# Kernel optimization log

Measured on AMD Instinct MI355X. Metric: run time of the kernel, lower is better.

Reference implementation:

```python
import jax, jax.numpy as jnp
import numpy as np

N_NODES = 50000
N_EDGES = 800000
IN_FEATS = 256
OUT_FEATS = 128


def setup_inputs() -> dict:
    key = jax.random.key(0)
    k1, k2, k3, k4 = jax.random.split(key, 4)
    feat = jax.random.normal(k1, (N_NODES, IN_FEATS), dtype=jnp.float32)
    # xavier uniform init for weight [in, out]
    limit = float(np.sqrt(6.0 / (IN_FEATS + OUT_FEATS)))
    weight = jax.random.uniform(k2, (IN_FEATS, OUT_FEATS), minval=-limit, maxval=limit, dtype=jnp.float32)
    bias = jnp.zeros((OUT_FEATS,), dtype=jnp.float32)
    src = jax.random.randint(k3, (N_EDGES,), 0, N_NODES, dtype=jnp.int32)
    dst = jax.random.randint(k4, (N_EDGES,), 0, N_NODES, dtype=jnp.int32)
    return {"feat": feat, "weight": weight, "bias": bias, "src": src, "dst": dst}


def reference(feat, weight, bias, src, dst):
    N = feat.shape[0]
    in_f, out_f = weight.shape
    # right normalization: 1 / out_degree(src node), clamped to >= 1
    deg = jax.ops.segment_sum(jnp.ones(src.shape[0], dtype=feat.dtype), src, num_segments=N)
    norm = (1.0 / jnp.maximum(deg, 1.0))[:, None]  # [N,1]
    if in_f > out_f:
        # transform first (cheaper messages), then normalize + aggregate
        h = jnp.matmul(feat, weight) * norm          # [N, out]
        rst = jax.ops.segment_sum(h[src], dst, num_segments=N)  # scatter-sum over edges
    else:
        h = feat * norm                               # [N, in]
        rst = jax.ops.segment_sum(h[src], dst, num_segments=N)
        rst = jnp.matmul(rst, weight)
    return rst + bias
```

## Files before the change

kernel.cpp:

```cpp
#include <hip/hip_runtime.h>

#define N_NODES 50000
#define N_EDGES 800000
#define IN_F 256
#define OUT_F 128

#define CHUNKS 128
#define EPC (N_EDGES / CHUNKS)
#define BINW (N_NODES / 4)
#define NWORDS (N_NODES / 4)
#define RGB 196
#define HIST_BLOCKS (2 * CHUNKS)
#define CPW8 (CHUNKS / 8)

#define GEMMF_BLOCKS 196
#define HEPC (EPC / 2)

typedef __attribute__((ext_vector_type(8))) short short8;
typedef __attribute__((ext_vector_type(4))) float float4_t;

__device__ __forceinline__ short f2bf(float f) {
  unsigned u = __builtin_bit_cast(unsigned, f);
  u = u + 0x7FFFu + ((u >> 16) & 1u);
  return (short)(u >> 16);
}

__device__ __forceinline__ float bflo(unsigned u) {
  return __builtin_bit_cast(float, u << 16);
}
__device__ __forceinline__ float bfhi(unsigned u) {
  return __builtin_bit_cast(float, u & 0xFFFF0000u);
}


__global__ __launch_bounds__(512) void hist_kernel(const int* __restrict__ src,
                                                   const int* __restrict__ dst,
                                                   unsigned char* __restrict__ pdst8,
                                                   unsigned char* __restrict__ psrc8,
                                                   unsigned char* __restrict__ rank8,
                                                   int* __restrict__ cursor) {
  __shared__ unsigned bins[BINW];
  int b = blockIdx.x;
  int tid = threadIdx.x;
  if (b == 0 && tid == 0) *cursor = 0;
  int hs = b >> 7;
  int c = b & 127;
  uint4* b4 = (uint4*)bins;
  for (int j = tid; j < BINW / 4; j += 512) b4[j] = (uint4){0u, 0u, 0u, 0u};
  __syncthreads();
  const int* key = hs ? src : dst;
  int e0 = c * EPC;

  auto process = [&](int v, int eI) {
    unsigned sh = (v & 3) * 8;
    unsigned old = atomicAdd(&bins[v >> 2], 1u << sh);
    if (!hs) rank8[eI] = (unsigned char)((old >> sh) & 0xFFu);
  };

#pragma unroll 2
  for (int tile = 0; tile < 3; ++tile) {
    int i = tile * 2048 + tid;
    int k0 = key[e0 + i];
    int k1 = key[e0 + i + 512];
    int k2 = key[e0 + i + 1024];
    int k3 = key[e0 + i + 1536];
    process(k0, e0 + i);
    process(k1, e0 + i + 512);
    process(k2, e0 + i + 1024);
    process(k3, e0 + i + 1536);
  }
  {
    int i = 6144 + tid;
    if (i < EPC) process(key[e0 + i], e0 + i);
  }
  __syncthreads();
  uint4* p128 = (uint4*)((hs ? psrc8 : pdst8) + (size_t)c * N_NODES);
  const uint4* s128 = (const uint4*)bins;
  for (int j = tid; j < BINW / 4; j += 512) p128[j] = s128[j];
}

__global__ __launch_bounds__(512) void gemmred_kernel(const float* __restrict__ feat,
                                                      const float* __restrict__ W,
                                                      unsigned short* __restrict__ h,
                                                      const unsigned char* __restrict__ pdst8,
                                                      const unsigned char* __restrict__ psrc8,
                                                      unsigned char* __restrict__ delta8,
                                                      int* __restrict__ cnt,
                                                      int* __restrict__ row_start,
                                                      int* __restrict__ cursor,
                                                      float* __restrict__ norm) {
  __shared__ uint4 smem4[4096];
  int b = blockIdx.x;
  int tid = threadIdx.x;

  if (b < GEMMF_BLOCKS) {
    short* wl = (short*)smem4;
#pragma unroll
    for (int i = 0; i < 64; ++i) {
      int idx = i * 512 + tid;
      int k = idx >> 7, n = idx & 127;
      int s = k >> 5, q = (k >> 3) & 3, j = k & 7;
      int tt = n >> 4, m = n & 15;
      wl[((s * 8 + tt) * 64 + q * 16 + m) * 8 + j] = f2bf(W[idx]);
    }
    __syncthreads();

    int w = tid >> 6, l = tid & 63;
    int m = l & 15, q = l >> 4;
    long base = (long)b * 256 + w * 32;

    float4_t acc[2][8];
#pragma unroll
    for (int r = 0; r < 2; ++r)
#pragma unroll
      for (int to = 0; to < 8; ++to) acc[r][to] = (float4_t)(0.0f);

    long row0 = base + m;
    long row1 = base + 16 + m;
    long r0c = row0 < N_NODES - 1 ? row0 : N_NODES - 1;
    long r1c = row1 < N_NODES - 1 ? row1 : N_NODES - 1;
    const float* a0p = feat + (size_t)r0c * IN_F;
    const float* a1p = feat + (size_t)r1c * IN_F;
    const short8* wl8 = (const short8*)smem4;

#pragma unroll
    for (int s = 0; s < 8; ++s) {
      int k0 = s * 32 + q * 8;
      float4_t av0a = *(const float4_t*)(a0p + k0);
      float4_t av0b = *(const float4_t*)(a0p + k0 + 4);
      float4_t av1a = *(const float4_t*)(a1p + k0);
      float4_t av1b = *(const float4_t*)(a1p + k0 + 4);
      short8 fa0, fa1;
#pragma unroll
      for (int i = 0; i < 4; ++i) {
        fa0[i] = f2bf(av0a[i]);
        fa0[i + 4] = f2bf(av0b[i]);
        fa1[i] = f2bf(av1a[i]);
        fa1[i + 4] = f2bf(av1b[i]);
      }
#pragma unroll
      for (int to = 0; to < 8; ++to) {
        short8 fb = wl8[(s * 8 + to) * 64 + l];
        acc[0][to] = __builtin_amdgcn_mfma_f32_16x16x32_bf16(fa0, fb, acc[0][to], 0, 0, 0);
        acc[1][to] = __builtin_amdgcn_mfma_f32_16x16x32_bf16(fa1, fb, acc[1][to], 0, 0, 0);
      }
    }

#pragma unroll
    for (int r = 0; r < 2; ++r) {
#pragma unroll
      for (int i = 0; i < 4; ++i) {
        long row = base + r * 16 + q * 4 + i;
        if (row < N_NODES) {
          short8 hv;
#pragma unroll
          for (int to = 0; to < 8; ++to) hv[to] = f2bf(acc[r][to][i]);
          *(short8*)(h + (size_t)row * OUT_F + m * 8) = hv;
        }
      }
    }
    return;
  }

  int rb = b - GEMMF_BLOCKS;
  int side = rb >= RGB ? 1 : 0;
  int g = rb - side * RGB;
  int w = tid >> 6, l = tid & 63;
  int wd = g * 64 + l;
  bool ok = wd < NWORDS;
  int wdc = ok ? wd : NWORDS - 1;
  const unsigned* P = (const unsigned*)(side == 0 ? pdst8 : psrc8);
  unsigned(*tot)[64] = (unsigned(*)[64])smem4;

  unsigned vals[CPW8];
  unsigned s = 0;
#pragma unroll
  for (int i = 0; i < CPW8; ++i) {
    vals[i] = P[(size_t)(w * CPW8 + i) * NWORDS + wdc];
    s += vals[i];
  }
  tot[w][l] = s;
  __syncthreads();

  if (side == 0) {
    unsigned base = 0;
#pragma unroll
    for (int w2 = 0; w2 < 8; ++w2)
      if (w2 < w) base += tot[w2][l];
    unsigned run = base;
    unsigned* D = (unsigned*)delta8;
    if (ok) {
#pragma unroll
      for (int i = 0; i < CPW8; ++i) {
        D[(size_t)(w * CPW8 + i) * NWORDS + wd] = run;
        run += vals[i];
      }
    }
    if (w == 0) {
      unsigned ftot = 0;
#pragma unroll
      for (int w2 = 0; w2 < 8; ++w2) ftot += tot[w2][l];
      if (!ok) ftot = 0;
      int c0 = ftot & 255, c1 = (ftot >> 8) & 255, c2 = (ftot >> 16) & 255, c3 = ftot >> 24;
      int T = c0 + c1 + c2 + c3;
      int x = T;
#pragma unroll
      for (int off = 1; off < 64; off <<= 1) {
        int y = __shfl_up(x, off);
        if (l >= off) x += y;
      }
      int waveTotal = __shfl(x, 63);
      int sb = 0;
      if (l == 63) sb = atomicAdd(cursor, waveTotal);
      sb = __shfl(sb, 63);
      int E = sb + x - T;
      if (ok) {
        int4 cv = {c0, c1, c2, c3};
        int4 rv = {E, E + c0, E + c0 + c1, E + c0 + c1 + c2};
        ((int4*)cnt)[wd] = cv;
        ((int4*)row_start)[wd] = rv;
      }
    }
  } else {
    if (w == 0 && ok) {
      unsigned ftot = 0;
#pragma unroll
      for (int w2 = 0; w2 < 8; ++w2) ftot += tot[w2][l];
      float4 nv;
      int d0 = ftot & 255, d1 = (ftot >> 8) & 255, d2 = (ftot >> 16) & 255, d3 = (int)(ftot >> 24);
      nv.x = 1.0f / (float)(d0 > 1 ? d0 : 1);
      nv.y = 1.0f / (float)(d1 > 1 ? d1 : 1);
      nv.z = 1.0f / (float)(d2 > 1 ? d2 : 1);
      nv.w = 1.0f / (float)(d3 > 1 ? d3 : 1);
      ((float4*)norm)[wd] = nv;
    }
  }
}

__global__ __launch_bounds__(512) void scat_kernel(const int* __restrict__ src,
                                                   const int* __restrict__ dst,
                                                   const int* __restrict__ row_start,
                                                   const unsigned char* __restrict__ delta8,
                                                   const unsigned char* __restrict__ rank8,
                                                   int* __restrict__ eidx) {
  __shared__ uint4 dl4[N_NODES / 16];
  int b = blockIdx.x;
  int tid = threadIdx.x;
  int c = b >> 1, hb = b & 1;
  const uint4* rowp = (const uint4*)(delta8 + (size_t)c * N_NODES);
  for (int j = tid; j < N_NODES / 16; j += 512) dl4[j] = rowp[j];
  __syncthreads();
  const unsigned char* dl = (const unsigned char*)dl4;
  int e0 = c * EPC + hb * HEPC;

  int dsts[6], rks[6], srcs[6], rss[6];
#pragma unroll
  for (int k = 0; k < 6; ++k) {
    int e = e0 + k * 512 + tid;
    dsts[k] = dst[e];
    rks[k] = (int)rank8[e];
  }
#pragma unroll
  for (int k = 0; k < 6; ++k) rss[k] = row_start[dsts[k]];
#pragma unroll
  for (int k = 0; k < 6; ++k) srcs[k] = src[e0 + k * 512 + tid];
#pragma unroll
  for (int k = 0; k < 6; ++k) {
    int pos = rss[k] + (int)dl[dsts[k]] + rks[k];
    eidx[pos] = srcs[k];
  }
  if (tid < HEPC - 6 * 512) {
    int e = e0 + 3072 + tid;
    int d = dst[e];
    int pos = row_start[d] + (int)dl[d] + (int)rank8[e];
    eidx[pos] = src[e];
  }
}

__global__ __launch_bounds__(256) void agg_kernel(const unsigned short* __restrict__ h,
                                                  const int* __restrict__ row_start,
                                                  const int* __restrict__ cnt,
                                                  const int* __restrict__ eidx,
                                                  const float* __restrict__ norm,
                                                  const float* __restrict__ bias,
                                                  float* __restrict__ out) {
  int w = threadIdx.x >> 6, l = threadIdx.x & 63;
  int d = blockIdx.x * 4 + w;
  int rs = row_start[d], re = rs + cnt[d];
  const uint4* __restrict__ hu4 = (const uint4*)h;
  int rowsel = l >> 4;
  int cp = l & 15;
  float a0 = 0.f, a1 = 0.f, a2 = 0.f, a3 = 0.f, a4 = 0.f, a5 = 0.f, a6 = 0.f, a7 = 0.f;

  auto acc8 = [&](uint4 v, float nm) {
    a0 = fmaf(bflo(v.x), nm, a0); a1 = fmaf(bfhi(v.x), nm, a1);
    a2 = fmaf(bflo(v.y), nm, a2); a3 = fmaf(bfhi(v.y), nm, a3);
    a4 = fmaf(bflo(v.z), nm, a4); a5 = fmaf(bfhi(v.z), nm, a5);
    a6 = fmaf(bflo(v.w), nm, a6); a7 = fmaf(bfhi(v.w), nm, a7);
  };

  for (int bse = rs; bse < re; bse += 64) {
    int n = re - bse; if (n > 64) n = 64;
    int e = (l < n) ? eidx[bse + l] : 0;
    int quarter = (n + 3) >> 2;
    int j = 0;
    for (; j + 4 <= quarter; j += 4) {
      int i0 = 4 * j + rowsel;
      int s0 = __shfl(e, i0);
      int s1 = __shfl(e, i0 + 4);
      int s2 = __shfl(e, i0 + 8);
      int s3 = __shfl(e, i0 + 12);
      uint4 v0 = hu4[(size_t)s0 * 16 + cp];
      uint4 v1 = hu4[(size_t)s1 * 16 + cp];
      uint4 v2 = hu4[(size_t)s2 * 16 + cp];
      uint4 v3 = hu4[(size_t)s3 * 16 + cp];
      float nm0 = norm[s0], nm1 = norm[s1], nm2 = norm[s2], nm3 = norm[s3];
      if (i0 >= n) v0 = (uint4){0u, 0u, 0u, 0u};
      if (i0 + 4 >= n) v1 = (uint4){0u, 0u, 0u, 0u};
      if (i0 + 8 >= n) v2 = (uint4){0u, 0u, 0u, 0u};
      if (i0 + 12 >= n) v3 = (uint4){0u, 0u, 0u, 0u};
      acc8(v0, nm0);
      acc8(v1, nm1);
      acc8(v2, nm2);
      acc8(v3, nm3);
    }
    for (; j < quarter; ++j) {
      int i0 = 4 * j + rowsel;
      int s0 = __shfl(e, i0);
      uint4 v0 = hu4[(size_t)s0 * 16 + cp];
      float nm0 = norm[s0];
      if (i0 >= n) v0 = (uint4){0u, 0u, 0u, 0u};
      acc8(v0, nm0);
    }
  }
  a0 += __shfl_xor(a0, 16); a1 += __shfl_xor(a1, 16);
  a2 += __shfl_xor(a2, 16); a3 += __shfl_xor(a3, 16);
  a4 += __shfl_xor(a4, 16); a5 += __shfl_xor(a5, 16);
  a6 += __shfl_xor(a6, 16); a7 += __shfl_xor(a7, 16);
  a0 += __shfl_xor(a0, 32); a1 += __shfl_xor(a1, 32);
  a2 += __shfl_xor(a2, 32); a3 += __shfl_xor(a3, 32);
  a4 += __shfl_xor(a4, 32); a5 += __shfl_xor(a5, 32);
  a6 += __shfl_xor(a6, 32); a7 += __shfl_xor(a7, 32);
  if (rowsel == 0) {
    float av[8] = {a0, a1, a2, a3, a4, a5, a6, a7};
    float* op = out + (size_t)d * OUT_F;
#pragma unroll
    for (int j = 0; j < 8; ++j) {
      int col = j * 16 + cp;
      op[col] = av[j] + bias[col];
    }
  }
}

extern "C" void kernel_launch(void* const* d_in, const int* in_sizes, int n_in,
                              void* d_out, int out_size, void* d_ws, size_t ws_size,
                              hipStream_t stream) {
  const float* feat = (const float*)d_in[0];
  const float* weight = (const float*)d_in[1];
  const float* bias = (const float*)d_in[2];
  const int* src = (const int*)d_in[3];
  const int* dst = (const int*)d_in[4];
  float* out = (float*)d_out;

  char* ws = (char*)d_ws;
  size_t off = 0;
  auto alloc = [&](size_t bytes) -> void* {
    void* p = ws + off;
    off += (bytes + 511) & ~(size_t)511;
    return p;
  };
  int* cursor = (int*)alloc(4);
  int* cnt = (int*)alloc(N_NODES * 4);
  int* row_start = (int*)alloc(N_NODES * 4);
  float* norm = (float*)alloc(N_NODES * 4);
  int* eidx = (int*)alloc(N_EDGES * 4);
  unsigned short* h = (unsigned short*)alloc((size_t)N_NODES * OUT_F * 2);
  unsigned char* pdst8 = (unsigned char*)alloc((size_t)CHUNKS * N_NODES);
  unsigned char* psrc8 = (unsigned char*)alloc((size_t)CHUNKS * N_NODES);
  unsigned char* delta8 = (unsigned char*)alloc((size_t)CHUNKS * N_NODES);
  unsigned char* rank8 = (unsigned char*)alloc((size_t)N_EDGES);
  (void)off; (void)ws_size; (void)in_sizes; (void)n_in; (void)out_size;

  hipLaunchKernelGGL(hist_kernel, dim3(HIST_BLOCKS), dim3(512), 0, stream,
                     src, dst, pdst8, psrc8, rank8, cursor);
  hipLaunchKernelGGL(gemmred_kernel, dim3(GEMMF_BLOCKS + 2 * RGB), dim3(512), 0, stream,
                     feat, weight, h, pdst8, psrc8, delta8, cnt, row_start, cursor, norm);
  hipLaunchKernelGGL(scat_kernel, dim3(2 * CHUNKS), dim3(512), 0, stream,
                     src, dst, row_start, delta8, rank8, eidx);
  hipLaunchKernelGGL(agg_kernel, dim3(N_NODES / 4), dim3(256), 0, stream,
                     h, row_start, cnt, eidx, norm, bias, out);
}
```

Before: 161.9 us.

## Split GEMM blocks across histogram and reduction kernels to overlap work

The dense feature GEMM blocks are moved into a shared device function. Half of them now run alongside the histogram blocks in the first kernel and the other half alongside the prefix-reduction blocks in the second kernel, instead of all running in the second kernel. This spreads compute-bound GEMM work over both launches so it can fill CUs left idle by the memory/atomic-bound histogram phase. The cost is that the histogram kernel now uses the larger 64KB shared-memory footprint, which may reduce its occupancy.

```diff
diff --git a/kernel.cpp b/kernel.cpp
--- a/kernel.cpp
+++ b/kernel.cpp
@@ -14,6 +14,8 @@
 #define CPW8 (CHUNKS / 8)
 
 #define GEMMF_BLOCKS 196
+#define GEMM_K1 98
+#define GEMM_K2 98
 #define HEPC (EPC / 2)
 
 typedef __attribute__((ext_vector_type(8))) short short8;
@@ -33,15 +35,97 @@
 }
 
 
-__global__ __launch_bounds__(512) void hist_kernel(const int* __restrict__ src,
-                                                   const int* __restrict__ dst,
-                                                   unsigned char* __restrict__ pdst8,
-                                                   unsigned char* __restrict__ psrc8,
-                                                   unsigned char* __restrict__ rank8,
-                                                   int* __restrict__ cursor) {
-  __shared__ unsigned bins[BINW];
+__device__ __forceinline__ void gemm_block(int gb, int tid,
+                                           const float* __restrict__ feat,
+                                           const float* __restrict__ W,
+                                           unsigned short* __restrict__ h,
+                                           uint4* smem4) {
+  short* wl = (short*)smem4;
+#pragma unroll
+  for (int i = 0; i < 64; ++i) {
+    int idx = i * 512 + tid;
+    int k = idx >> 7, n = idx & 127;
+    int s = k >> 5, q = (k >> 3) & 3, j = k & 7;
+    int tt = n >> 4, m = n & 15;
+    wl[((s * 8 + tt) * 64 + q * 16 + m) * 8 + j] = f2bf(W[idx]);
+  }
+  __syncthreads();
+
+  int w = tid >> 6, l = tid & 63;
+  int m = l & 15, q = l >> 4;
+  long base = (long)gb * 256 + w * 32;
+
+  float4_t acc[2][8];
+#pragma unroll
+  for (int r = 0; r < 2; ++r)
+#pragma unroll
+    for (int to = 0; to < 8; ++to) acc[r][to] = (float4_t)(0.0f);
+
+  long row0 = base + m;
+  long row1 = base + 16 + m;
+  long r0c = row0 < N_NODES - 1 ? row0 : N_NODES - 1;
+  long r1c = row1 < N_NODES - 1 ? row1 : N_NODES - 1;
+  const float* a0p = feat + (size_t)r0c * IN_F;
+  const float* a1p = feat + (size_t)r1c * IN_F;
+  const short8* wl8 = (const short8*)smem4;
+
+#pragma unroll
+  for (int s = 0; s < 8; ++s) {
+    int k0 = s * 32 + q * 8;
+    float4_t av0a = *(const float4_t*)(a0p + k0);
+    float4_t av0b = *(const float4_t*)(a0p + k0 + 4);
+    float4_t av1a = *(const float4_t*)(a1p + k0);
+    float4_t av1b = *(const float4_t*)(a1p + k0 + 4);
+    short8 fa0, fa1;
+#pragma unroll
+    for (int i = 0; i < 4; ++i) {
+      fa0[i] = f2bf(av0a[i]);
+      fa0[i + 4] = f2bf(av0b[i]);
+      fa1[i] = f2bf(av1a[i]);
+      fa1[i + 4] = f2bf(av1b[i]);
+    }
+#pragma unroll
+    for (int to = 0; to < 8; ++to) {
+      short8 fb = wl8[(s * 8 + to) * 64 + l];
+      acc[0][to] = __builtin_amdgcn_mfma_f32_16x16x32_bf16(fa0, fb, acc[0][to], 0, 0, 0);
+      acc[1][to] = __builtin_amdgcn_mfma_f32_16x16x32_bf16(fa1, fb, acc[1][to], 0, 0, 0);
+    }
+  }
+
+#pragma unroll
+  for (int r = 0; r < 2; ++r) {
+#pragma unroll
+    for (int i = 0; i < 4; ++i) {
+      long row = base + r * 16 + q * 4 + i;
+      if (row < N_NODES) {
+        short8 hv;
+#pragma unroll
+        for (int to = 0; to < 8; ++to) hv[to] = f2bf(acc[r][to][i]);
+        *(short8*)(h + (size_t)row * OUT_F + m * 8) = hv;
+      }
+    }
+  }
+}
+
+__global__ __launch_bounds__(512) void histgemm_kernel(const int* __restrict__ src,
+                                                       const int* __restrict__ dst,
+                                                       unsigned char* __restrict__ pdst8,
+                                                       unsigned char* __restrict__ psrc8,
+                                                       unsigned char* __restrict__ rank8,
+                                                       int* __restrict__ cursor,
+                                                       const float* __restrict__ feat,
+                                                       const float* __restrict__ W,
+                                                       unsigned short* __restrict__ h) {
+  __shared__ uint4 smem4[4096];
   int b = blockIdx.x;
   int tid = threadIdx.x;
+
+  if (b >= HIST_BLOCKS) {
+    gemm_block(b - HIST_BLOCKS, tid, feat, W, h, smem4);
+    return;
+  }
+
+  unsigned* bins = (unsigned*)smem4;
   if (b == 0 && tid == 0) *cursor = 0;
   int hs = b >> 7;
   int c = b & 127;
@@ -75,11 +159,11 @@
   }
   __syncthreads();
   uint4* p128 = (uint4*)((hs ? psrc8 : pdst8) + (size_t)c * N_NODES);
-  const uint4* s128 = (const uint4*)bins;
+  const uint4* s128 = (const uint4*)smem4;
   for (int j = tid; j < BINW / 4; j += 512) p128[j] = s128[j];
 }
 
-__global__ __launch_bounds__(512) void gemmred_kernel(const float* __restrict__ feat,
+__global__ __launch_bounds__(512) void redgemm_kernel(const float* __restrict__ feat,
                                                       const float* __restrict__ W,
                                                       unsigned short* __restrict__ h,
                                                       const unsigned char* __restrict__ pdst8,
@@ -93,78 +177,13 @@
   int b = blockIdx.x;
   int tid = threadIdx.x;
 
-  if (b < GEMMF_BLOCKS) {
-    short* wl = (short*)smem4;
-#pragma unroll
-    for (int i = 0; i < 64; ++i) {
-      int idx = i * 512 + tid;
-      int k = idx >> 7, n = idx & 127;
-      int s = k >> 5, q = (k >> 3) & 3, j = k & 7;
-      int tt = n >> 4, m = n & 15;
-      wl[((s * 8 + tt) * 64 + q * 16 + m) * 8 + j] = f2bf(W[idx]);
-    }
-    __syncthreads();
-
-    int w = tid >> 6, l = tid & 63;
-    int m = l & 15, q = l >> 4;
-    long base = (long)b * 256 + w * 32;
-
-    float4_t acc[2][8];
-#pragma unroll
-    for (int r = 0; r < 2; ++r)
-#pragma unroll
-      for (int to = 0; to < 8; ++to) acc[r][to] = (float4_t)(0.0f);
-
-    long row0 = base + m;
-    long row1 = base + 16 + m;
-    long r0c = row0 < N_NODES - 1 ? row0 : N_NODES - 1;
-    long r1c = row1 < N_NODES - 1 ? row1 : N_NODES - 1;
-    const float* a0p = feat + (size_t)r0c * IN_F;
-    const float* a1p = feat + (size_t)r1c * IN_F;
-    const short8* wl8 = (const short8*)smem4;
-
-#pragma unroll
-    for (int s = 0; s < 8; ++s) {
-      int k0 = s * 32 + q * 8;
-      float4_t av0a = *(const float4_t*)(a0p + k0);
-      float4_t av0b = *(const float4_t*)(a0p + k0 + 4);
-      float4_t av1a = *(const float4_t*)(a1p + k0);
-      float4_t av1b = *(const float4_t*)(a1p + k0 + 4);
-      short8 fa0, fa1;
-#pragma unroll
-      for (int i = 0; i < 4; ++i) {
-        fa0[i] = f2bf(av0a[i]);
-        fa0[i + 4] = f2bf(av0b[i]);
-        fa1[i] = f2bf(av1a[i]);
-        fa1[i + 4] = f2bf(av1b[i]);
-      }
-#pragma unroll
-      for (int to = 0; to < 8; ++to) {
-        short8 fb = wl8[(s * 8 + to) * 64 + l];
-        acc[0][to] = __builtin_amdgcn_mfma_f32_16x16x32_bf16(fa0, fb, acc[0][to], 0, 0, 0);
-        acc[1][to] = __builtin_amdgcn_mfma_f32_16x16x32_bf16(fa1, fb, acc[1][to], 0, 0, 0);
-      }
-    }
-
-#pragma unroll
-    for (int r = 0; r < 2; ++r) {
-#pragma unroll
-      for (int i = 0; i < 4; ++i) {
-        long row = base + r * 16 + q * 4 + i;
-        if (row < N_NODES) {
-          short8 hv;
-#pragma unroll
-          for (int to = 0; to < 8; ++to) hv[to] = f2bf(acc[r][to][i]);
-          *(short8*)(h + (size_t)row * OUT_F + m * 8) = hv;
-        }
-      }
-    }
+  if (b >= 2 * RGB) {
+    gemm_block(GEMM_K1 + (b - 2 * RGB), tid, feat, W, h, smem4);
     return;
   }
 
-  int rb = b - GEMMF_BLOCKS;
-  int side = rb >= RGB ? 1 : 0;
-  int g = rb - side * RGB;
+  int side = b >= RGB ? 1 : 0;
+  int g = b - side * RGB;
   int w = tid >> 6, l = tid & 63;
   int wd = g * 64 + l;
   bool ok = wd < NWORDS;
@@ -381,9 +400,9 @@
   unsigned char* rank8 = (unsigned char*)alloc((size_t)N_EDGES);
   (void)off; (void)ws_size; (void)in_sizes; (void)n_in; (void)out_size;
 
-  hipLaunchKernelGGL(hist_kernel, dim3(HIST_BLOCKS), dim3(512), 0, stream,
-                     src, dst, pdst8, psrc8, rank8, cursor);
-  hipLaunchKernelGGL(gemmred_kernel, dim3(GEMMF_BLOCKS + 2 * RGB), dim3(512), 0, stream,
+  hipLaunchKernelGGL(histgemm_kernel, dim3(HIST_BLOCKS + GEMM_K1), dim3(512), 0, stream,
+                     src, dst, pdst8, psrc8, rank8, cursor, feat, weight, h);
+  hipLaunchKernelGGL(redgemm_kernel, dim3(2 * RGB + GEMM_K2), dim3(512), 0, stream,
                      feat, weight, h, pdst8, psrc8, delta8, cnt, row_start, cursor, norm);
   hipLaunchKernelGGL(scat_kernel, dim3(2 * CHUNKS), dim3(512), 0, stream,
                      src, dst, row_start, delta8, rank8, eidx);
```

Result: slower. 177.8 us (+9.8%).
